# Kernel optimization log

Hardware: AMD Instinct MI355X
Metric: run time of the kernel (lower is better)

The kernel has to match this reference:

```python
import jax, jax.numpy as jnp
import numpy as np

H = 128          # image_size
FOCAL = 3.0      # camera focal length (NDC scale)
ZNEAR = 1e-2
EPS = 1e-8

def setup_inputs() -> dict:
    key = jax.random.key(0)
    k1, k2, k3, k4 = jax.random.split(key, 4)
    B, V, F = 2, 2048, 512
    verts_world = jax.random.uniform(k1, (B, V, 3), minval=-1.0, maxval=1.0, dtype=jnp.float32)
    faces = jax.random.randint(k2, (F, 3), 0, V)
    R = jnp.tile(jnp.eye(3, dtype=jnp.float32)[None], (B, 1, 1)) + 0.05 * jax.random.normal(k3, (B, 3, 3), dtype=jnp.float32)
    # camera sits 4 units back so all geometry has positive view-space depth
    T = jnp.concatenate([0.1 * jax.random.normal(k4, (B, 2), dtype=jnp.float32), jnp.full((B, 1), 4.0, jnp.float32)], axis=-1)
    return {"verts_world": verts_world, "faces": faces, "R": R, "T": T}

def _seg_d2(px, py, ax, ay, bx, by):
    # squared distance from point (px,py) to segment (a,b)
    abx, aby = bx - ax, by - ay
    apx, apy = px - ax, py - ay
    t = jnp.clip((apx * abx + apy * aby) / (abx * abx + aby * aby + EPS), 0.0, 1.0)
    dx, dy = apx - t * abx, apy - t * aby
    return dx * dx + dy * dy

def _project(verts_world, R, T):
    # world -> view (row-vector convention, as pytorch3d transform_points)
    v_view = jnp.einsum('bvj,bjk->bvk', verts_world, R) + T[:, None, :]
    z = v_view[..., 2:3]                       # view-space depth kept as screen z (as in MeshRasterizer.transform)
    xy = FOCAL * v_view[..., :2] / z           # perspective projection to NDC
    return jnp.concatenate([xy, z], axis=-1)   # [B,V,3]

def _rasterize(verts_ndc, faces):
    tri = verts_ndc[:, faces]                  # [B,F,3,3]
    def c(i, j):
        return tri[:, :, i, j][:, None, None, :]   # [B,1,1,F]
    x0, y0, z0 = c(0, 0), c(0, 1), c(0, 2)
    x1, y1, z1 = c(1, 0), c(1, 1), c(1, 2)
    x2, y2, z2 = c(2, 0), c(2, 1), c(2, 2)
    # pixel centers, pytorch3d NDC convention (+X left, +Y up)
    s = 1.0 - (2.0 * jnp.arange(H, dtype=verts_ndc.dtype) + 1.0) / H
    px = s[None, None, :, None]                # varies over W
    py = s[None, :, None, None]                # varies over H
    area = (x1 - x0) * (y2 - y0) - (y1 - y0) * (x2 - x0)      # 2 * signed area
    denom = jnp.where(jnp.abs(area) > EPS, area, EPS)
    w0 = ((x2 - x1) * (py - y1) - (y2 - y1) * (px - x1)) / denom
    w1 = ((x0 - x2) * (py - y2) - (y0 - y2) * (px - x2)) / denom
    w2 = 1.0 - w0 - w1                         # barycentrics [B,H,W,F]
    inside = (w0 >= 0) & (w1 >= 0) & (w2 >= 0)
    zp = w0 * z0 + w1 * z1 + w2 * z2           # barycentric-interpolated depth
    valid = inside & (zp > ZNEAR) & (jnp.abs(area) > EPS)
    d2 = jnp.minimum(_seg_d2(px, py, x0, y0, x1, y1),
                     jnp.minimum(_seg_d2(px, py, x1, y1, x2, y2),
                                 _seg_d2(px, py, x2, y2, x0, y0)))
    dists = jnp.where(inside, -d2, d2)         # signed squared edge distance
    zsort = jnp.where(valid, zp, jnp.inf)
    idx = jnp.argmin(zsort, axis=-1)           # nearest covering face per pixel (faces_per_pixel=1)
    hit = jnp.isfinite(jnp.min(zsort, axis=-1))
    take = lambda a: jnp.take_along_axis(a, idx[..., None], axis=-1)[..., 0]
    zbuf = jnp.where(hit, take(zp), -1.0)
    bary = jnp.stack([take(w0), take(w1), take(w2)], axis=-1)
    bary = jnp.where(hit[..., None], bary, -1.0)
    dsel = jnp.where(hit, take(dists), -1.0)
    pix_to_face = jnp.where(hit, idx, -1)
    # trailing K=1 (faces_per_pixel) dim, matching Fragments layout
    return pix_to_face[..., None], zbuf[..., None], bary[:, :, :, None, :], dsel[..., None]

def reference(verts_world, faces, R, T):
    verts_ndc = _project(verts_world, R, T)
    return _rasterize(verts_ndc, faces)
```

## Files before the change

### kernel.cpp

```cpp
#include <hip/hip_runtime.h>
#include <cstdint>

#define H_ 128
#define V_ 2048
#define F_ 512
#define B_ 2
#define FOCAL_ 3.0f
#define ZNEAR_ 0.01f
#define EPS_ 1e-8f
#define PAD_ 1e-3f

__global__ __launch_bounds__(1024) void k_prep(const float* __restrict__ vw,
                                               const int* __restrict__ faces,
                                               const float* __restrict__ R,
                                               const float* __restrict__ T,
                                               float* __restrict__ fd,
                                               float4* __restrict__ bb) {
  __shared__ float ndc[B_ * V_ * 3];
  int t = threadIdx.x;

  for (int tid = t; tid < B_ * V_; tid += 1024) {
    int b = tid >> 11;
    const float* v  = vw + tid * 3;
    const float* Rb = R + b * 9;
    const float* Tb = T + b * 3;
    float vx = v[0], vy = v[1], vz = v[2];
    float o[3];
#pragma unroll
    for (int k = 0; k < 3; ++k) {
      float a = __fadd_rn(__fadd_rn(__fmul_rn(vx, Rb[k]), __fmul_rn(vy, Rb[3 + k])),
                          __fmul_rn(vz, Rb[6 + k]));
      o[k] = __fadd_rn(a, Tb[k]);
    }
    float z = o[2];
    ndc[tid * 3 + 0] = __fdiv_rn(__fmul_rn(FOCAL_, o[0]), z);
    ndc[tid * 3 + 1] = __fdiv_rn(__fmul_rn(FOCAL_, o[1]), z);
    ndc[tid * 3 + 2] = z;
  }
  __syncthreads();

  {
    int tid = t;
    int b = tid >> 9;
    int f = tid & (F_ - 1);
    int i0 = faces[f * 3 + 0], i1 = faces[f * 3 + 1], i2 = faces[f * 3 + 2];
    const float* nb = ndc + b * V_ * 3;
    float x0 = nb[i0 * 3], y0 = nb[i0 * 3 + 1], z0 = nb[i0 * 3 + 2];
    float x1 = nb[i1 * 3], y1 = nb[i1 * 3 + 1], z1 = nb[i1 * 3 + 2];
    float x2 = nb[i2 * 3], y2 = nb[i2 * 3 + 1], z2 = nb[i2 * 3 + 2];
    float area = __fsub_rn(__fmul_rn(__fsub_rn(x1, x0), __fsub_rn(y2, y0)),
                           __fmul_rn(__fsub_rn(y1, y0), __fsub_rn(x2, x0)));
    bool ok = fabsf(area) > EPS_;
    float denom = ok ? area : EPS_;
    float* o = fd + tid * 16;
    o[0]  = x1;  o[1]  = y1;  o[2]  = x2;  o[3]  = y2;
    o[4]  = z0;  o[5]  = z1;  o[6]  = z2;  o[7]  = denom;
    o[8]  = __fsub_rn(x2, x1);  o[9]  = __fsub_rn(y2, y1);
    o[10] = __fsub_rn(x0, x2);  o[11] = __fsub_rn(y0, y2);
    o[12] = x0;  o[13] = y0;  o[14] = ok ? 1.0f : 0.0f;  o[15] = 0.0f;
    float4 box;
    if (ok) {
      box.x = fminf(fminf(x0, x1), x2) - PAD_;
      box.y = fmaxf(fmaxf(x0, x1), x2) + PAD_;
      box.z = fminf(fminf(y0, y1), y2) - PAD_;
      box.w = fmaxf(fmaxf(y0, y1), y2) + PAD_;
    } else {
      box.x = 1e30f; box.y = -1e30f; box.z = 1e30f; box.w = -1e30f;
    }
    bb[tid] = box;
  }
}

__device__ __forceinline__ float seg_d2(float px, float py, float ax, float ay,
                                        float bx, float by) {
  float abx = __fsub_rn(bx, ax), aby = __fsub_rn(by, ay);
  float apx = __fsub_rn(px, ax), apy = __fsub_rn(py, ay);
  float num = __fadd_rn(__fmul_rn(apx, abx), __fmul_rn(apy, aby));
  float den = __fadd_rn(__fadd_rn(__fmul_rn(abx, abx), __fmul_rn(aby, aby)), EPS_);
  float t = __fdiv_rn(num, den);
  t = fminf(fmaxf(t, 0.0f), 1.0f);
  float dx = __fsub_rn(apx, __fmul_rn(t, abx));
  float dy = __fsub_rn(apy, __fmul_rn(t, aby));
  return __fadd_rn(__fmul_rn(dx, dx), __fmul_rn(dy, dy));
}

__global__ __launch_bounds__(512) void k_raster(const float* __restrict__ fd,
                                                const float4* __restrict__ bb,
                                                float* __restrict__ out) {
  __shared__ float lf[F_ * 16];
  __shared__ float4 lbb[F_];
  __shared__ unsigned long long red[64 * 8];
  int blk = blockIdx.x;
  int b  = blk >> 8;
  int iy = (blk >> 1) & (H_ - 1);
  int h  = blk & 1;
  int t = threadIdx.x;
  int lane = t & 63;
  int q = t >> 6;
  int ix = h * 64 + lane;

  const float4* src = (const float4*)(fd + b * F_ * 16);
  float4* dst = (float4*)lf;
  for (int i = t; i < F_ * 4; i += 512) dst[i] = src[i];
  for (int i = t; i < F_; i += 512) lbb[i] = bb[b * F_ + i];
  __syncthreads();

  float px = 1.0f - (float)(2 * ix + 1) * 0.0078125f;
  float py = 1.0f - (float)(2 * iy + 1) * 0.0078125f;
  const float INF = __int_as_float(0x7f800000);
  float best = INF;
  int bidx = q * 64;

#pragma unroll 2
  for (int f = q * 64; f < q * 64 + 64; ++f) {
    float4 box = lbb[f];
    bool cull = (px < box.x) || (px > box.y) || (py < box.z) || (py > box.w);
    if (__all(cull)) continue;
    const float* Fp = &lf[f * 16];
    float x1 = Fp[0], y1 = Fp[1], x2 = Fp[2], y2 = Fp[3];
    float z0 = Fp[4], z1 = Fp[5], z2 = Fp[6], denom = Fp[7];
    float dx21 = Fp[8], dy21 = Fp[9], dx02 = Fp[10], dy02 = Fp[11];
    float aok = Fp[14];
    float w0 = __fdiv_rn(__fsub_rn(__fmul_rn(dx21, __fsub_rn(py, y1)),
                                   __fmul_rn(dy21, __fsub_rn(px, x1))), denom);
    float w1 = __fdiv_rn(__fsub_rn(__fmul_rn(dx02, __fsub_rn(py, y2)),
                                   __fmul_rn(dy02, __fsub_rn(px, x2))), denom);
    float w2 = __fsub_rn(__fsub_rn(1.0f, w0), w1);
    float zp = __fadd_rn(__fadd_rn(__fmul_rn(w0, z0), __fmul_rn(w1, z1)),
                         __fmul_rn(w2, z2));
    bool valid = (w0 >= 0.0f) && (w1 >= 0.0f) && (w2 >= 0.0f) &&
                 (zp > ZNEAR_) && (aok > 0.5f);
    float zs = valid ? zp : INF;
    if (zs < best) { best = zs; bidx = f; }
  }

  red[lane * 8 + q] =
      ((unsigned long long)__float_as_uint(best) << 32) | (unsigned long long)(unsigned)bidx;
  __syncthreads();

  if (q == 0) {
    unsigned long long m = red[lane * 8];
#pragma unroll
    for (int j = 1; j < 8; ++j) {
      unsigned long long v = red[lane * 8 + j];
      m = (v < m) ? v : m;
    }
    unsigned zb = (unsigned)(m >> 32);
    int idx = (int)(m & 0xffffffffu);
    bool hit = zb < 0x7f800000u;

    const float* Fp = &lf[idx * 16];
    float x1 = Fp[0], y1 = Fp[1], x2 = Fp[2], y2 = Fp[3];
    float z0 = Fp[4], z1 = Fp[5], z2 = Fp[6], denom = Fp[7];
    float dx21 = Fp[8], dy21 = Fp[9], dx02 = Fp[10], dy02 = Fp[11];
    float x0 = Fp[12], y0 = Fp[13];
    float w0 = __fdiv_rn(__fsub_rn(__fmul_rn(dx21, __fsub_rn(py, y1)),
                                   __fmul_rn(dy21, __fsub_rn(px, x1))), denom);
    float w1 = __fdiv_rn(__fsub_rn(__fmul_rn(dx02, __fsub_rn(py, y2)),
                                   __fmul_rn(dy02, __fsub_rn(px, x2))), denom);
    float w2 = __fsub_rn(__fsub_rn(1.0f, w0), w1);
    float zp = __fadd_rn(__fadd_rn(__fmul_rn(w0, z0), __fmul_rn(w1, z1)),
                         __fmul_rn(w2, z2));
    float d01 = seg_d2(px, py, x0, y0, x1, y1);
    float d12 = seg_d2(px, py, x1, y1, x2, y2);
    float d20 = seg_d2(px, py, x2, y2, x0, y0);
    float d2 = fminf(d01, fminf(d12, d20));

    int pix = ((b * H_ + iy) * H_) + ix;
    out[pix]                 = hit ? (float)idx : -1.0f;
    out[32768 + pix]         = hit ? zp : -1.0f;
    out[65536 + pix * 3 + 0] = hit ? w0 : -1.0f;
    out[65536 + pix * 3 + 1] = hit ? w1 : -1.0f;
    out[65536 + pix * 3 + 2] = hit ? w2 : -1.0f;
    out[163840 + pix]        = hit ? -d2 : -1.0f;
  }
}

extern "C" void kernel_launch(void* const* d_in, const int* in_sizes, int n_in,
                              void* d_out, int out_size, void* d_ws, size_t ws_size,
                              hipStream_t stream) {
  const float* vw    = (const float*)d_in[0];
  const int*   faces = (const int*)d_in[1];
  const float* R     = (const float*)d_in[2];
  const float* T     = (const float*)d_in[3];
  float* out = (float*)d_out;
  float* ws  = (float*)d_ws;
  float*  fd  = ws;
  float4* bbp = (float4*)(ws + 16384);
  k_prep<<<1, 1024, 0, stream>>>(vw, faces, R, T, fd, bbp);
  k_raster<<<512, 512, 0, stream>>>(fd, bbp, out);
}
```

Before: 91.69 us.

## Ballot-compact face culling per wavefront and defer divisions behind edge sign test

```diff
diff --git a/kernel.cpp b/kernel.cpp
--- a/kernel.cpp
+++ b/kernel.cpp
@@ -87,9 +87,9 @@
 __global__ __launch_bounds__(512) void k_raster(const float* __restrict__ fd,
                                                 const float4* __restrict__ bb,
                                                 float* __restrict__ out) {
-  __shared__ float lf[F_ * 16];
-  __shared__ float4 lbb[F_];
+  __shared__ float4 lf4[F_ * 4];
   __shared__ unsigned long long red[64 * 8];
+  const float* lf = (const float*)lf4;
   int blk = blockIdx.x;
   int b  = blk >> 8;
   int iy = (blk >> 1) & (H_ - 1);
@@ -100,38 +100,45 @@
   int ix = h * 64 + lane;
 
   const float4* src = (const float4*)(fd + b * F_ * 16);
-  float4* dst = (float4*)lf;
-  for (int i = t; i < F_ * 4; i += 512) dst[i] = src[i];
-  for (int i = t; i < F_; i += 512) lbb[i] = bb[b * F_ + i];
+  for (int i = t; i < F_ * 4; i += 512) lf4[i] = src[i];
   __syncthreads();
 
   float px = 1.0f - (float)(2 * ix + 1) * 0.0078125f;
   float py = 1.0f - (float)(2 * iy + 1) * 0.0078125f;
+  float pxmax = 1.0f - (float)(2 * (h * 64) + 1) * 0.0078125f;
+  float pxmin = 1.0f - (float)(2 * (h * 64 + 63) + 1) * 0.0078125f;
+
+  float4 box = bb[b * F_ + q * 64 + lane];
+  bool ov = (box.x <= pxmax) && (box.y >= pxmin) && (box.z <= py) && (box.w >= py);
+  unsigned long long m = __ballot(ov);
+
   const float INF = __int_as_float(0x7f800000);
   float best = INF;
   int bidx = q * 64;
 
-#pragma unroll 2
-  for (int f = q * 64; f < q * 64 + 64; ++f) {
-    float4 box = lbb[f];
-    bool cull = (px < box.x) || (px > box.y) || (py < box.z) || (py > box.w);
-    if (__all(cull)) continue;
-    const float* Fp = &lf[f * 16];
-    float x1 = Fp[0], y1 = Fp[1], x2 = Fp[2], y2 = Fp[3];
-    float z0 = Fp[4], z1 = Fp[5], z2 = Fp[6], denom = Fp[7];
-    float dx21 = Fp[8], dy21 = Fp[9], dx02 = Fp[10], dy02 = Fp[11];
-    float aok = Fp[14];
-    float w0 = __fdiv_rn(__fsub_rn(__fmul_rn(dx21, __fsub_rn(py, y1)),
-                                   __fmul_rn(dy21, __fsub_rn(px, x1))), denom);
-    float w1 = __fdiv_rn(__fsub_rn(__fmul_rn(dx02, __fsub_rn(py, y2)),
-                                   __fmul_rn(dy02, __fsub_rn(px, x2))), denom);
-    float w2 = __fsub_rn(__fsub_rn(1.0f, w0), w1);
-    float zp = __fadd_rn(__fadd_rn(__fmul_rn(w0, z0), __fmul_rn(w1, z1)),
-                         __fmul_rn(w2, z2));
-    bool valid = (w0 >= 0.0f) && (w1 >= 0.0f) && (w2 >= 0.0f) &&
-                 (zp > ZNEAR_) && (aok > 0.5f);
-    float zs = valid ? zp : INF;
-    if (zs < best) { best = zs; bidx = f; }
+  while (m) {
+    int f = q * 64 + __builtin_ctzll(m);
+    m &= m - 1;
+    float4 q0 = lf4[f * 4 + 0];
+    float4 q1 = lf4[f * 4 + 1];
+    float4 q2 = lf4[f * 4 + 2];
+    float e0 = __fsub_rn(__fmul_rn(q2.x, __fsub_rn(py, q0.y)),
+                         __fmul_rn(q2.y, __fsub_rn(px, q0.x)));
+    float e1 = __fsub_rn(__fmul_rn(q2.z, __fsub_rn(py, q0.w)),
+                         __fmul_rn(q2.w, __fsub_rn(px, q0.z)));
+    bool dpos = q1.w > 0.0f;
+    bool s0 = dpos ? (e0 >= 0.0f) : (e0 <= 0.0f);
+    bool s1 = dpos ? (e1 >= 0.0f) : (e1 <= 0.0f);
+    if (__any(s0 && s1)) {
+      float w0 = __fdiv_rn(e0, q1.w);
+      float w1 = __fdiv_rn(e1, q1.w);
+      float w2 = __fsub_rn(__fsub_rn(1.0f, w0), w1);
+      float zp = __fadd_rn(__fadd_rn(__fmul_rn(w0, q1.x), __fmul_rn(w1, q1.y)),
+                           __fmul_rn(w2, q1.z));
+      bool valid = s0 && s1 && (w2 >= 0.0f) && (zp > ZNEAR_);
+      float zs = valid ? zp : INF;
+      if (zs < best) { best = zs; bidx = f; }
+    }
   }
 
   red[lane * 8 + q] =
@@ -139,14 +146,14 @@
   __syncthreads();
 
   if (q == 0) {
-    unsigned long long m = red[lane * 8];
+    unsigned long long mm = red[lane * 8];
 #pragma unroll
     for (int j = 1; j < 8; ++j) {
       unsigned long long v = red[lane * 8 + j];
-      m = (v < m) ? v : m;
+      mm = (v < mm) ? v : mm;
     }
-    unsigned zb = (unsigned)(m >> 32);
-    int idx = (int)(m & 0xffffffffu);
+    unsigned zb = (unsigned)(mm >> 32);
+    int idx = (int)(mm & 0xffffffffu);
     bool hit = zb < 0x7f800000u;
 
     const float* Fp = &lf[idx * 16];
```

After: 84.43 us. -7.9%, faster.
